# Kernel tuning notes

Hardware: AMD Instinct MI355X
Metric: run time of the kernel (lower is better)

## Reference

```python
import jax, jax.numpy as jnp
import numpy as np

E, M, K, N = 32, 1024, 512, 512

def setup_inputs() -> dict:
    key = jax.random.key(0)
    k1, k2, k3 = jax.random.split(key, 3)
    A = jax.random.normal(k1, (E, M, K), dtype=jnp.float32)
    B = jax.random.normal(k2, (E, N, K), dtype=jnp.float32)
    expert_num_tokens = jax.random.randint(k3, (E,), 0, M + 1, dtype=jnp.int32)
    return {"A": A, "B": B, "expert_num_tokens": expert_num_tokens}

def reference(A, B, expert_num_tokens):
    # Per-expert GEMM: C[e] = A[e] @ B[e].T  -> [E, M, N]
    C = jnp.einsum('emk,enk->emn', A, B)
    # Rows m >= expert_num_tokens[e] are never computed/stored by the kernel;
    # zero them in the reference output.
    row_valid = jnp.arange(A.shape[1])[None, :] < expert_num_tokens[:, None]  # [E, M]
    return jnp.where(row_valid[:, :, None], C, jnp.zeros((), C.dtype))
```

## Files before the change

kernel.cpp:

```cpp
#include <hip/hip_runtime.h>
#include <hip/hip_bf16.h>

#define NE 32
#define MM 1024
#define KK 512
#define NN 512
#define BM 128
#define BN 128
#define BK 32

typedef __attribute__((ext_vector_type(8))) short bf16x8;
typedef __attribute__((ext_vector_type(4))) float floatx4;

__device__ __forceinline__ short f2bf(float f) {
  union { __hip_bfloat16 b; short s; } u;
  u.b = __float2bfloat16(f);
  return u.s;
}

extern "C" __global__ __launch_bounds__(256, 4)
void expert_gemm(const float* __restrict__ A, const float* __restrict__ B,
                 const int* __restrict__ cnts, float* __restrict__ C)
{
  const int xcd  = blockIdx.x & 7;
  const int slot = blockIdx.x >> 3;
  const int tid  = threadIdx.x;

  int e = -1, mt = 0, nt = 0;
  int acc = 0;
#pragma unroll
  for (int g = 0; g < 4; ++g) {
    int ee = xcd + (g << 3);
    int vt = (cnts[ee] + BM - 1) >> 7;
    int c4 = vt << 2;
    if (e < 0 && slot < acc + c4) { int r = slot - acc; e = ee; mt = r >> 2; nt = r & 3; }
    acc += c4;
  }
  if (e < 0) {
    int z = slot - acc, a2 = 0;
#pragma unroll
    for (int g = 0; g < 4; ++g) {
      int ee = xcd + (g << 3);
      int vt = (cnts[ee] + BM - 1) >> 7;
      int c = 8 - vt;
      if (e < 0 && z < a2 + c) { e = ee; mt = vt + (z - a2); }
      a2 += c;
    }
    if (e < 0) return;
    float* Ce = C + ((size_t)e * MM + mt * BM) * NN;
    float4 zf = make_float4(0.f, 0.f, 0.f, 0.f);
#pragma unroll
    for (int i = 0; i < 64; ++i) {
      int fidx = i * 256 + tid;
      int r = fidx >> 7, c = (fidx & 127) << 2;
      *(float4*)(Ce + (size_t)r * NN + c) = zf;
    }
    return;
  }

  const int m0 = mt * BM, n0 = nt * BN;
  const int cnt = cnts[e];
  const float* Ae = A + ((size_t)e * MM + m0) * KK;
  const float* Be = B + ((size_t)e * NN + n0) * KK;
  float* Ce = C + ((size_t)e * MM + m0) * NN + n0;

  __shared__ __align__(16) short lA[BM * BK];
  __shared__ __align__(16) short lB[BN * BK];

  const int wave = tid >> 6, lane = tid & 63;
  const int wm = (wave >> 1) * 64, wn = (wave & 1) * 64;
  const int fr = lane & 15, kh = lane >> 4;

  const int srow = tid >> 2;
  const int su   = tid & 3;

  floatx4 acc4[4][4] = {};

  float4 pa0[2], pa1[2], pb0[2], pb1[2];
#pragma unroll
  for (int p = 0; p < 2; ++p) {
    int row = srow + (p << 6);
    int col = su << 3;
    pa0[p] = *(const float4*)(Ae + (size_t)row * KK + col);
    pa1[p] = *(const float4*)(Ae + (size_t)row * KK + col + 4);
    pb0[p] = *(const float4*)(Be + (size_t)row * KK + col);
    pb1[p] = *(const float4*)(Be + (size_t)row * KK + col + 4);
  }

  for (int kt = 0; kt < KK; kt += BK) {
    __syncthreads();
#pragma unroll
    for (int p = 0; p < 2; ++p) {
      int row = srow + (p << 6);
      int unit = (row << 2) + (su ^ (row & 3));
      bf16x8 va = { f2bf(pa0[p].x), f2bf(pa0[p].y), f2bf(pa0[p].z), f2bf(pa0[p].w),
                    f2bf(pa1[p].x), f2bf(pa1[p].y), f2bf(pa1[p].z), f2bf(pa1[p].w) };
      bf16x8 vb = { f2bf(pb0[p].x), f2bf(pb0[p].y), f2bf(pb0[p].z), f2bf(pb0[p].w),
                    f2bf(pb1[p].x), f2bf(pb1[p].y), f2bf(pb1[p].z), f2bf(pb1[p].w) };
      *(bf16x8*)(lA + (unit << 3)) = va;
      *(bf16x8*)(lB + (unit << 3)) = vb;
    }
    __syncthreads();

    if (kt + BK < KK) {
#pragma unroll
      for (int p = 0; p < 2; ++p) {
        int row = srow + (p << 6);
        int col = kt + BK + (su << 3);
        pa0[p] = *(const float4*)(Ae + (size_t)row * KK + col);
        pa1[p] = *(const float4*)(Ae + (size_t)row * KK + col + 4);
        pb0[p] = *(const float4*)(Be + (size_t)row * KK + col);
        pb1[p] = *(const float4*)(Be + (size_t)row * KK + col + 4);
      }
    }

    bf16x8 af[4], bfv[4];
#pragma unroll
    for (int i = 0; i < 4; ++i) {
      int rA = wm + (i << 4) + fr;
      af[i]  = *(const bf16x8*)(lA + ((((rA << 2) + (kh ^ (rA & 3)))) << 3));
      int rB = wn + (i << 4) + fr;
      bfv[i] = *(const bf16x8*)(lB + ((((rB << 2) + (kh ^ (rB & 3)))) << 3));
    }
#pragma unroll
    for (int i = 0; i < 4; ++i)
#pragma unroll
      for (int j = 0; j < 4; ++j)
        acc4[i][j] = __builtin_amdgcn_mfma_f32_16x16x32_bf16(af[i], bfv[j], acc4[i][j], 0, 0, 0);
  }

  const int rb_ = (lane >> 4) * 4;
#pragma unroll
  for (int i = 0; i < 4; ++i) {
#pragma unroll
    for (int r = 0; r < 4; ++r) {
      int row = wm + i * 16 + rb_ + r;
      bool valid = (m0 + row) < cnt;
#pragma unroll
      for (int j = 0; j < 4; ++j) {
        int col = wn + j * 16 + fr;
        Ce[(size_t)row * NN + col] = valid ? acc4[i][j][r] : 0.0f;
      }
    }
  }
}

extern "C" void kernel_launch(void* const* d_in, const int* in_sizes, int n_in,
                              void* d_out, int out_size, void* d_ws, size_t ws_size,
                              hipStream_t stream) {
  const float* A    = (const float*)d_in[0];
  const float* B    = (const float*)d_in[1];
  const int*   cnts = (const int*)d_in[2];
  float*       C    = (float*)d_out;

  hipLaunchKernelGGL(expert_gemm, dim3(1024), dim3(256), 0, stream, A, B, cnts, C);
}
```

Baseline: 171.3 us.

## Double-buffer LDS tiles, drop XCD mapping, order zero-fill blocks first

Splits the shared-memory A/B tiles into two buffers so each k-step needs one barrier instead of two, and adds a scheduling barrier so the next global loads are issued before the MFMA work. Block scheduling drops the XCD-aware expert grouping: zero-fill blocks now come first in block order, followed by GEMM tiles enumerated across all experts. Launch bounds drop from 4 to 3 blocks per CU to fit the doubled LDS and registers. Occupancy falls and L2 locality per expert may change.

```diff
diff --git a/kernel.cpp b/kernel.cpp
--- a/kernel.cpp
+++ b/kernel.cpp
@@ -8,6 +8,7 @@
 #define BM 128
 #define BN 128
 #define BK 32
+#define NS (KK / BK)
 
 typedef __attribute__((ext_vector_type(8))) short bf16x8;
 typedef __attribute__((ext_vector_type(4))) float floatx4;
@@ -18,35 +19,23 @@
   return u.s;
 }
 
-extern "C" __global__ __launch_bounds__(256, 4)
+extern "C" __global__ __launch_bounds__(256, 3)
 void expert_gemm(const float* __restrict__ A, const float* __restrict__ B,
                  const int* __restrict__ cnts, float* __restrict__ C)
 {
-  const int xcd  = blockIdx.x & 7;
-  const int slot = blockIdx.x >> 3;
-  const int tid  = threadIdx.x;
+  const int b   = blockIdx.x;
+  const int tid = threadIdx.x;
 
   int e = -1, mt = 0, nt = 0;
   int acc = 0;
-#pragma unroll
-  for (int g = 0; g < 4; ++g) {
-    int ee = xcd + (g << 3);
-    int vt = (cnts[ee] + BM - 1) >> 7;
-    int c4 = vt << 2;
-    if (e < 0 && slot < acc + c4) { int r = slot - acc; e = ee; mt = r >> 2; nt = r & 3; }
-    acc += c4;
+#pragma unroll 1
+  for (int i = 0; i < NE; ++i) {
+    int vt = (cnts[i] + BM - 1) >> 7;
+    int c = 8 - vt;
+    if (e < 0 && b < acc + c) { e = i; mt = vt + (b - acc); }
+    acc += c;
   }
-  if (e < 0) {
-    int z = slot - acc, a2 = 0;
-#pragma unroll
-    for (int g = 0; g < 4; ++g) {
-      int ee = xcd + (g << 3);
-      int vt = (cnts[ee] + BM - 1) >> 7;
-      int c = 8 - vt;
-      if (e < 0 && z < a2 + c) { e = ee; mt = vt + (z - a2); }
-      a2 += c;
-    }
-    if (e < 0) return;
+  if (e >= 0) {
     float* Ce = C + ((size_t)e * MM + mt * BM) * NN;
     float4 zf = make_float4(0.f, 0.f, 0.f, 0.f);
 #pragma unroll
@@ -57,6 +46,16 @@
     }
     return;
   }
+  int g = b - acc;
+  acc = 0;
+#pragma unroll 1
+  for (int i = 0; i < NE; ++i) {
+    int vt = (cnts[i] + BM - 1) >> 7;
+    int c4 = vt << 2;
+    if (e < 0 && g < acc + c4) { int r = g - acc; e = i; mt = r >> 2; nt = r & 3; }
+    acc += c4;
+  }
+  if (e < 0) return;
 
   const int m0 = mt * BM, n0 = nt * BN;
   const int cnt = cnts[e];
@@ -64,13 +63,12 @@
   const float* Be = B + ((size_t)e * NN + n0) * KK;
   float* Ce = C + ((size_t)e * MM + m0) * NN + n0;
 
-  __shared__ __align__(16) short lA[BM * BK];
-  __shared__ __align__(16) short lB[BN * BK];
+  __shared__ __align__(16) short lA[2][BM * BK];
+  __shared__ __align__(16) short lB[2][BN * BK];
 
   const int wave = tid >> 6, lane = tid & 63;
   const int wm = (wave >> 1) * 64, wn = (wave & 1) * 64;
   const int fr = lane & 15, kh = lane >> 4;
-
   const int srow = tid >> 2;
   const int su   = tid & 3;
 
@@ -87,8 +85,11 @@
     pb1[p] = *(const float4*)(Be + (size_t)row * KK + col + 4);
   }
 
-  for (int kt = 0; kt < KK; kt += BK) {
-    __syncthreads();
+#pragma unroll 1
+  for (int s = 0; s < NS; ++s) {
+    short* bufA = &lA[s & 1][0];
+    short* bufB = &lB[s & 1][0];
+
 #pragma unroll
     for (int p = 0; p < 2; ++p) {
       int row = srow + (p << 6);
@@ -97,30 +98,31 @@
                     f2bf(pa1[p].x), f2bf(pa1[p].y), f2bf(pa1[p].z), f2bf(pa1[p].w) };
       bf16x8 vb = { f2bf(pb0[p].x), f2bf(pb0[p].y), f2bf(pb0[p].z), f2bf(pb0[p].w),
                     f2bf(pb1[p].x), f2bf(pb1[p].y), f2bf(pb1[p].z), f2bf(pb1[p].w) };
-      *(bf16x8*)(lA + (unit << 3)) = va;
-      *(bf16x8*)(lB + (unit << 3)) = vb;
+      *(bf16x8*)(bufA + (unit << 3)) = va;
+      *(bf16x8*)(bufB + (unit << 3)) = vb;
     }
     __syncthreads();
 
-    if (kt + BK < KK) {
+    if (s + 1 < NS) {
+      int col = (s + 1) * BK + (su << 3);
 #pragma unroll
       for (int p = 0; p < 2; ++p) {
         int row = srow + (p << 6);
-        int col = kt + BK + (su << 3);
         pa0[p] = *(const float4*)(Ae + (size_t)row * KK + col);
         pa1[p] = *(const float4*)(Ae + (size_t)row * KK + col + 4);
         pb0[p] = *(const float4*)(Be + (size_t)row * KK + col);
         pb1[p] = *(const float4*)(Be + (size_t)row * KK + col + 4);
       }
     }
+    __builtin_amdgcn_sched_barrier(0);
 
     bf16x8 af[4], bfv[4];
 #pragma unroll
     for (int i = 0; i < 4; ++i) {
       int rA = wm + (i << 4) + fr;
-      af[i]  = *(const bf16x8*)(lA + ((((rA << 2) + (kh ^ (rA & 3)))) << 3));
+      af[i]  = *(const bf16x8*)(bufA + ((((rA << 2) + (kh ^ (rA & 3)))) << 3));
       int rB = wn + (i << 4) + fr;
-      bfv[i] = *(const bf16x8*)(lB + ((((rB << 2) + (kh ^ (rB & 3)))) << 3));
+      bfv[i] = *(const bf16x8*)(bufB + ((((rB << 2) + (kh ^ (rB & 3)))) << 3));
     }
 #pragma unroll
     for (int i = 0; i < 4; ++i)
```

Measured after the change: 160.3 us. 1.07x faster.

## Stage fp32 tiles via direct global-to-LDS loads and convert to bf16 after LDS read

Applied to the files above, without the earlier changes.

Replaces the register-prefetch path (global load into registers, convert to bf16, store to LDS) with global_load_lds DMA that writes raw fp32 tiles straight into LDS using an XOR swizzle. The bf16 conversion moves to the point where the MFMA operands are read from LDS, and BK doubles to 64, giving 64 KB of LDS per block and a launch-bounds occupancy hint of 2. The goal is to free VGPRs and cut VALU/LDS-store traffic. The cost is that the software prefetch overlap is lost: each k-step now waits on its DMA before computing. A 4x4 fragment is converted redundantly by both waves sharing it, and fewer blocks fit per CU.

```diff
diff --git a/kernel.cpp b/kernel.cpp
--- a/kernel.cpp
+++ b/kernel.cpp
@@ -7,7 +7,8 @@
 #define NN 512
 #define BM 128
 #define BN 128
-#define BK 32
+#define BK 64
+#define NS (KK / BK)
 
 typedef __attribute__((ext_vector_type(8))) short bf16x8;
 typedef __attribute__((ext_vector_type(4))) float floatx4;
@@ -18,7 +19,13 @@
   return u.s;
 }
 
-extern "C" __global__ __launch_bounds__(256, 4)
+__device__ __forceinline__ void dma16(const float* g, float* l) {
+  __builtin_amdgcn_global_load_lds(
+      (const __attribute__((address_space(1))) unsigned int*)g,
+      (__attribute__((address_space(3))) unsigned int*)l, 16, 0, 0);
+}
+
+extern "C" __global__ __launch_bounds__(256, 2)
 void expert_gemm(const float* __restrict__ A, const float* __restrict__ B,
                  const int* __restrict__ cnts, float* __restrict__ C)
 {
@@ -64,69 +71,54 @@
   const float* Be = B + ((size_t)e * NN + n0) * KK;
   float* Ce = C + ((size_t)e * MM + m0) * NN + n0;
 
-  __shared__ __align__(16) short lA[BM * BK];
-  __shared__ __align__(16) short lB[BN * BK];
+  __shared__ __align__(16) float sA[BM * BK];
+  __shared__ __align__(16) float sB[BN * BK];
 
   const int wave = tid >> 6, lane = tid & 63;
   const int wm = (wave >> 1) * 64, wn = (wave & 1) * 64;
   const int fr = lane & 15, kh = lane >> 4;
-
-  const int srow = tid >> 2;
-  const int su   = tid & 3;
+  const int ld = lane >> 4;
+  const int lk = lane & 15;
 
   floatx4 acc4[4][4] = {};
 
-  float4 pa0[2], pa1[2], pb0[2], pb1[2];
+#pragma unroll 1
+  for (int s = 0; s < NS; ++s) {
+    const int kt = s * BK;
 #pragma unroll
-  for (int p = 0; p < 2; ++p) {
-    int row = srow + (p << 6);
-    int col = su << 3;
-    pa0[p] = *(const float4*)(Ae + (size_t)row * KK + col);
-    pa1[p] = *(const float4*)(Ae + (size_t)row * KK + col + 4);
-    pb0[p] = *(const float4*)(Be + (size_t)row * KK + col);
-    pb1[p] = *(const float4*)(Be + (size_t)row * KK + col + 4);
-  }
-
-  for (int kt = 0; kt < KK; kt += BK) {
-    __syncthreads();
-#pragma unroll
-    for (int p = 0; p < 2; ++p) {
-      int row = srow + (p << 6);
-      int unit = (row << 2) + (su ^ (row & 3));
-      bf16x8 va = { f2bf(pa0[p].x), f2bf(pa0[p].y), f2bf(pa0[p].z), f2bf(pa0[p].w),
-                    f2bf(pa1[p].x), f2bf(pa1[p].y), f2bf(pa1[p].z), f2bf(pa1[p].w) };
-      bf16x8 vb = { f2bf(pb0[p].x), f2bf(pb0[p].y), f2bf(pb0[p].z), f2bf(pb0[p].w),
-                    f2bf(pb1[p].x), f2bf(pb1[p].y), f2bf(pb1[p].z), f2bf(pb1[p].w) };
-      *(bf16x8*)(lA + (unit << 3)) = va;
-      *(bf16x8*)(lB + (unit << 3)) = vb;
+    for (int q = 0; q < 8; ++q) {
+      int i   = wave * 8 + q;
+      int row = 4 * i + ld;
+      int kb  = lk ^ (row & 15);
+      dma16(Ae + (size_t)row * KK + kt + kb * 4, sA + i * 256);
+      dma16(Be + (size_t)row * KK + kt + kb * 4, sB + i * 256);
     }
     __syncthreads();
 
-    if (kt + BK < KK) {
 #pragma unroll
-      for (int p = 0; p < 2; ++p) {
-        int row = srow + (p << 6);
-        int col = kt + BK + (su << 3);
-        pa0[p] = *(const float4*)(Ae + (size_t)row * KK + col);
-        pa1[p] = *(const float4*)(Ae + (size_t)row * KK + col + 4);
-        pb0[p] = *(const float4*)(Be + (size_t)row * KK + col);
-        pb1[p] = *(const float4*)(Be + (size_t)row * KK + col + 4);
+    for (int ks = 0; ks < 2; ++ks) {
+      bf16x8 af[4], bfv[4];
+#pragma unroll
+      for (int i = 0; i < 4; ++i) {
+        int rA  = wm + (i << 4) + fr;
+        int kb0 = ks * 8 + kh * 2;
+        float4 f0 = *(const float4*)(sA + ((rA << 4) + (kb0 ^ (rA & 15))) * 4);
+        float4 f1 = *(const float4*)(sA + ((rA << 4) + ((kb0 + 1) ^ (rA & 15))) * 4);
+        af[i] = (bf16x8){ f2bf(f0.x), f2bf(f0.y), f2bf(f0.z), f2bf(f0.w),
+                          f2bf(f1.x), f2bf(f1.y), f2bf(f1.z), f2bf(f1.w) };
+        int rB  = wn + (i << 4) + fr;
+        float4 g0 = *(const float4*)(sB + ((rB << 4) + (kb0 ^ (rB & 15))) * 4);
+        float4 g1 = *(const float4*)(sB + ((rB << 4) + ((kb0 + 1) ^ (rB & 15))) * 4);
+        bfv[i] = (bf16x8){ f2bf(g0.x), f2bf(g0.y), f2bf(g0.z), f2bf(g0.w),
+                           f2bf(g1.x), f2bf(g1.y), f2bf(g1.z), f2bf(g1.w) };
       }
+#pragma unroll
+      for (int i = 0; i < 4; ++i)
+#pragma unroll
+        for (int j = 0; j < 4; ++j)
+          acc4[i][j] = __builtin_amdgcn_mfma_f32_16x16x32_bf16(af[i], bfv[j], acc4[i][j], 0, 0, 0);
     }
-
-    bf16x8 af[4], bfv[4];
-#pragma unroll
-    for (int i = 0; i < 4; ++i) {
-      int rA = wm + (i << 4) + fr;
-      af[i]  = *(const bf16x8*)(lA + ((((rA << 2) + (kh ^ (rA & 3)))) << 3));
-      int rB = wn + (i << 4) + fr;
-      bfv[i] = *(const bf16x8*)(lB + ((((rB << 2) + (kh ^ (rB & 3)))) << 3));
-    }
-#pragma unroll
-    for (int i = 0; i < 4; ++i)
-#pragma unroll
-      for (int j = 0; j < 4; ++j)
-        acc4[i][j] = __builtin_amdgcn_mfma_f32_16x16x32_bf16(af[i], bfv[j], acc4[i][j], 0, 0, 0);
+    __syncthreads();
   }
 
   const int rb_ = (lane >> 4) * 4;
```

Result: faster. 164.5 us (-4.0%).
